# Kernel optimization log

Hardware: AMD Instinct MI355X
Metric: run time of the kernel (lower is better)

The kernel has to match this reference:

```python
import jax, jax.numpy as jnp
import numpy as np

H, W, C = 64, 64, 64
B = 64
N_HEADS = 4
CONV_FILTERS = 64
BASIS_DIM = 16


def get_spatial_basis(h, w, d):
    half_d = d // 2
    basis = np.zeros((h, w, d), dtype=np.float32)
    div = np.exp(np.arange(0, half_d, 2, dtype=np.float32) * -np.log(100.0) / half_d)
    h_grid = np.expand_dims(np.arange(0, h, dtype=np.float32), 1)
    w_grid = np.expand_dims(np.arange(0, w, dtype=np.float32), 1)
    basis[:, :, 0:half_d:2] = np.sin(h_grid * div)[:, np.newaxis, :]
    basis[:, :, 1:half_d:2] = np.cos(h_grid * div)[:, np.newaxis, :]
    basis[:, :, half_d::2] = np.sin(w_grid * div)[np.newaxis, :, :]
    basis[:, :, half_d + 1::2] = np.cos(w_grid * div)[np.newaxis, :, :]
    return basis


def setup_inputs() -> dict:
    key = jax.random.key(0)
    ks = jax.random.split(key, 8)
    feat_in = C + BASIS_DIM  # 80 input channels for 1x1 convs
    return {
        "image": jax.random.normal(ks[0], (B, H, W, C), jnp.float32),
        "state1": jax.random.normal(ks[1], (B, 512), jnp.float32),
        "state2": jax.random.normal(ks[2], (B, 512), jnp.float32),
        "extra": jax.random.normal(ks[3], (B, 256), jnp.float32),
        "Wq": jax.random.normal(ks[4], (1024, CONV_FILTERS), jnp.float32) * 0.03,
        "bq": jnp.zeros((CONV_FILTERS,), jnp.float32),
        "Wk": jax.random.normal(ks[5], (feat_in, CONV_FILTERS), jnp.float32) * 0.1,
        "bk": jnp.zeros((CONV_FILTERS,), jnp.float32),
        "Wv": jax.random.normal(ks[6], (feat_in, CONV_FILTERS), jnp.float32) * 0.1,
        "bv": jnp.zeros((CONV_FILTERS,), jnp.float32),
        "spatial_basis": jnp.asarray(get_spatial_basis(H, W, BASIS_DIM)),
    }


def reference(image, state1, state2, extra, Wq, bq, Wk, bk, Wv, bv, spatial_basis):
    b, h, w, _ = image.shape
    nh = N_HEADS
    cf = Wq.shape[1]
    dph = cf // nh  # depth per head

    # concat image with tiled spatial basis -> [B,h,w,C+basis_dim]
    sb = jnp.broadcast_to(spatial_basis[None], (b,) + spatial_basis.shape)
    feats = jnp.concatenate([image, sb], axis=-1)

    # combiner over network-state tensors, then Dense query
    state = jnp.concatenate([state1, state2], axis=-1)  # [B,1024]
    q = state @ Wq + bq                                 # [B,cf]

    # 1x1 convs == per-pixel dense projections
    keys = feats @ Wk + bk    # [B,h,w,cf]
    vals = feats @ Wv + bv    # [B,h,w,cf]

    qh = q.reshape(b, nh, dph)
    kh = keys.reshape(b, h * w, nh, dph)
    vh = vals.reshape(b, h * w, nh, dph)

    # per-head dot scores over spatial positions, softmax over positions
    scores = jnp.einsum('bnd,bpnd->bpn', qh, kh)        # [B,hw,nh]
    attn = jax.nn.softmax(scores, axis=1)
    mean_attn = attn.mean(axis=-1).reshape(b, h, w)

    # weighted sum of values over spatial positions -> [B,cf]
    pooled = jnp.einsum('bpn,bpnd->bnd', attn, vh).reshape(b, cf)

    out = jnp.concatenate([pooled, extra], axis=-1)
    return out, mean_attn
```

## Files before the change

### kernel.cpp

```cpp
#include <hip/hip_runtime.h>
#include <hip/hip_bf16.h>

#define BATCH 64
#define HW    4096
#define PT    128
#define NS    32
#define FT_ST 136

#define FT_BASE  0
#define EST_BASE 10880
#define PR_BASE  13056
#define RED_BASE 15616
#define SMEM_TOT 15680

typedef unsigned int u32;
typedef unsigned short u16;
typedef __attribute__((ext_vector_type(8))) short bf16x8;
typedef __attribute__((ext_vector_type(4))) float f32x4;

__device__ __forceinline__ float bf2f(u16 h) { return __uint_as_float(((u32)h) << 16); }
__device__ __forceinline__ u32 f2bf(float x) {
  u32 b = __float_as_uint(x);
  return (b + 0x7fffu + ((b >> 16) & 1u)) >> 16;
}
__device__ __forceinline__ u32 pkbf(float lo, float hi) { return f2bf(lo) | (f2bf(hi) << 16); }

template<bool F32>
__device__ __forceinline__ float ld(const void* p, size_t i) {
  if (F32) return ((const float*)p)[i];
  return bf2f(((const u16*)p)[i]);
}
template<bool F32>
__device__ __forceinline__ void st(void* p, size_t i, float v) {
  if (F32) ((float*)p)[i] = v;
  else     ((__hip_bfloat16*)p)[i] = __float2bfloat16(v);
}

__device__ __forceinline__ bool detect_f32(const u16* __restrict__ image) {
  u16 h = image[(threadIdx.x & 63) * 2];
  u32 e = (h >> 7) & 0xFFu;
  unsigned long long m = __ballot(e >= 0x86u);
  return __popcll(m) >= 8;
}

__device__ __forceinline__ int swz(int c) { return ((c >> 3) & 3) << 3; }

template<bool F32>
__device__ void k1_body(const void* state1, const void* state2, const void* Wq, const void* bq,
                        const void* Wk, const void* bk, u16* weffbt, float* cb,
                        float* stt, float* qp, float* q) {
  const int b = blockIdx.x, tid = threadIdx.x;
  for (int i = tid; i < 512; i += 256) {
    stt[i]       = ld<F32>(state1, (size_t)b * 512 + i);
    stt[512 + i] = ld<F32>(state2, (size_t)b * 512 + i);
  }
  u32* wz = (u32*)(weffbt + (size_t)b * 1664);
  for (int i = tid; i < 832; i += 256) wz[i] = 0u;
  __syncthreads();
  {
    const int j = tid & 63, g = tid >> 6, i0 = g * 256;
    float a = 0.f;
#pragma unroll 8
    for (int i = 0; i < 256; ++i) a += stt[i0 + i] * ld<F32>(Wq, (size_t)(i0 + i) * 64 + j);
    qp[g * 64 + j] = a;
  }
  __syncthreads();
  if (tid < 64) q[tid] = qp[tid] + qp[64 + tid] + qp[128 + tid] + qp[192 + tid] + ld<F32>(bq, tid);
  __syncthreads();
  for (int t = tid; t < 320; t += 256) {
    const int c = t >> 2, n = t & 3;
    float a = 0.f;
#pragma unroll
    for (int d = 0; d < 16; ++d) a += ld<F32>(Wk, (size_t)c * 64 + n * 16 + d) * q[n * 16 + d];
    weffbt[(size_t)b * 1664 + n * 104 + c] = (u16)f2bf(a);
  }
  if (tid < 4) {
    float a = 0.f;
#pragma unroll
    for (int d = 0; d < 16; ++d) a += ld<F32>(bk, tid * 16 + d) * q[tid * 16 + d];
    cb[b * 4 + tid] = a;
  }
}

__global__ __launch_bounds__(256) void k1_prep(
    const void* image, const void* state1, const void* state2, const void* Wq, const void* bq,
    const void* Wk, const void* bk, u16* weffbt, float* cb) {
  __shared__ float stt[1024];
  __shared__ float qp[256];
  __shared__ float q[64];
  if (detect_f32((const u16*)image))
       k1_body<true >(state1, state2, Wq, bq, Wk, bk, weffbt, cb, stt, qp, q);
  else k1_body<false>(state1, state2, Wq, bq, Wk, bk, weffbt, cb, stt, qp, q);
}

__global__ __launch_bounds__(256, 4) void k2_main(
    const void* __restrict__ image, const void* __restrict__ basis,
    const float* __restrict__ cb, const u16* __restrict__ weffbt,
    u16* __restrict__ e_buf, float* __restrict__ m_blk, float* __restrict__ sum_blk,
    float* __restrict__ fpool_part) {
  __shared__ __align__(16) u16 smem[SMEM_TOT];
  float* redf  = (float*)(smem + RED_BASE);
  float* red2f = (float*)(smem + RED_BASE + 32);

  const int tid = threadIdx.x;
  const int b = blockIdx.x & 63, s = blockIdx.x >> 6;
  const int bs = b * NS + s;
  const int wave = tid >> 6, lane = tid & 63;
  const int m = lane & 15, q = lane >> 4;
  const bool isf32 = detect_f32((const u16*)image);

  if (isf32) {
    const float4* img4 = (const float4*)image + ((size_t)(b * HW + s * PT)) * 16;
#pragma unroll
    for (int i = 0; i < 4; ++i) {
      const int fidx = i * 256 + tid;
      const int pq = fidx >> 4, c4 = fidx & 15;
      const int ps = (pq * 2) ^ (((c4 >> 1) & 3) << 3);
      float4 v0 = img4[(pq * 2) * 16 + c4];
      float4 v1 = img4[(pq * 2 + 1) * 16 + c4];
      *(u32*)&smem[FT_BASE + (c4 * 4 + 0) * FT_ST + ps] = pkbf(v0.x, v1.x);
      *(u32*)&smem[FT_BASE + (c4 * 4 + 1) * FT_ST + ps] = pkbf(v0.y, v1.y);
      *(u32*)&smem[FT_BASE + (c4 * 4 + 2) * FT_ST + ps] = pkbf(v0.z, v1.z);
      *(u32*)&smem[FT_BASE + (c4 * 4 + 3) * FT_ST + ps] = pkbf(v0.w, v1.w);
    }
    const float4* bas4 = (const float4*)basis + (size_t)(s * PT) * 4;
    {
      const int pq = tid >> 2, c4 = tid & 3;
      const int ps = (pq * 2) ^ (((c4 >> 1) & 3) << 3);
      float4 v0 = bas4[(pq * 2) * 4 + c4];
      float4 v1 = bas4[(pq * 2 + 1) * 4 + c4];
      *(u32*)&smem[FT_BASE + (64 + c4 * 4 + 0) * FT_ST + ps] = pkbf(v0.x, v1.x);
      *(u32*)&smem[FT_BASE + (64 + c4 * 4 + 1) * FT_ST + ps] = pkbf(v0.y, v1.y);
      *(u32*)&smem[FT_BASE + (64 + c4 * 4 + 2) * FT_ST + ps] = pkbf(v0.z, v1.z);
      *(u32*)&smem[FT_BASE + (64 + c4 * 4 + 3) * FT_ST + ps] = pkbf(v0.w, v1.w);
    }
  } else {
    const uint4* img4 = (const uint4*)image + ((size_t)(b * HW + s * PT)) * 8;
#pragma unroll
    for (int i = 0; i < 2; ++i) {
      const int fidx = i * 256 + tid;
      const int pq = fidx >> 3, c8 = fidx & 7;
      const int ps = (pq * 2) ^ ((c8 & 3) << 3);
      uint4 u0 = img4[(pq * 2) * 8 + c8];
      uint4 u1 = img4[(pq * 2 + 1) * 8 + c8];
      const u32 w0[4] = {u0.x, u0.y, u0.z, u0.w};
      const u32 w1[4] = {u1.x, u1.y, u1.z, u1.w};
#pragma unroll
      for (int k = 0; k < 4; ++k) {
        *(u32*)&smem[FT_BASE + (c8 * 8 + 2 * k) * FT_ST + ps]     = (w0[k] & 0xffffu) | (w1[k] << 16);
        *(u32*)&smem[FT_BASE + (c8 * 8 + 2 * k + 1) * FT_ST + ps] = (w0[k] >> 16) | (w1[k] & 0xffff0000u);
      }
    }
    const uint4* bas4 = (const uint4*)basis + (size_t)(s * PT) * 2;
    if (tid < 128) {
      const int pq = tid >> 1, c8 = tid & 1;
      const int ps = (pq * 2) ^ ((c8 & 3) << 3);
      uint4 u0 = bas4[(pq * 2) * 2 + c8];
      uint4 u1 = bas4[(pq * 2 + 1) * 2 + c8];
      const u32 w0[4] = {u0.x, u0.y, u0.z, u0.w};
      const u32 w1[4] = {u1.x, u1.y, u1.z, u1.w};
#pragma unroll
      for (int k = 0; k < 4; ++k) {
        *(u32*)&smem[FT_BASE + (64 + c8 * 8 + 2 * k) * FT_ST + ps]     = (w0[k] & 0xffffu) | (w1[k] << 16);
        *(u32*)&smem[FT_BASE + (64 + c8 * 8 + 2 * k + 1) * FT_ST + ps] = (w0[k] >> 16) | (w1[k] & 0xffff0000u);
      }
    }
  }
  bf16x8 bfr[3];
  {
    const u16* wrow = weffbt + (size_t)b * 1664 + m * 104;
#pragma unroll
    for (int s3 = 0; s3 < 3; ++s3) bfr[s3] = *(const bf16x8*)&wrow[s3 * 32 + q * 8];
  }
  __syncthreads();

  f32x4 accS[2];
  {
    const float ci = (m < 4) ? cb[b * 4 + m] : 0.f;
#pragma unroll
    for (int t = 0; t < 2; ++t) { accS[t][0] = ci; accS[t][1] = ci; accS[t][2] = ci; accS[t][3] = ci; }
#pragma unroll
    for (int t = 0; t < 2; ++t) {
      const int pos = (wave * 2 + t) * 16 + m;
#pragma unroll
      for (int s3 = 0; s3 < 3; ++s3) {
        u32 aw[4];
        if (s3 == 2 && q >= 2) {
          aw[0] = aw[1] = aw[2] = aw[3] = 0u;
        } else {
#pragma unroll
          for (int jp = 0; jp < 4; ++jp) {
            const int c0 = s3 * 32 + q * 8 + jp * 2;
            const int ps = pos ^ swz(c0);
            u32 lo = smem[FT_BASE + c0 * FT_ST + ps];
            u32 hi = smem[FT_BASE + (c0 + 1) * FT_ST + ps];
            aw[jp] = lo | (hi << 16);
          }
        }
        accS[t] = __builtin_amdgcn_mfma_f32_16x16x32_bf16(*(const bf16x8*)aw, bfr[s3], accS[t], 0, 0, 0);
      }
    }
  }
  {
    float mx = accS[0][0];
#pragma unroll
    for (int t = 0; t < 2; ++t)
#pragma unroll
      for (int r = 0; r < 4; ++r) mx = fmaxf(mx, accS[t][r]);
    mx = fmaxf(mx, __shfl_xor(mx, 16, 64));
    mx = fmaxf(mx, __shfl_xor(mx, 32, 64));
    if (lane < 4) redf[wave * 4 + lane] = mx;
  }
  __syncthreads();

  float bmv;
  {
    const int hh = m & 3;
    bmv = fmaxf(fmaxf(redf[hh], redf[4 + hh]), fmaxf(redf[8 + hh], redf[12 + hh]));
  }
  {
    float ss = 0.f;
#pragma unroll
    for (int t = 0; t < 2; ++t) {
      const int T = wave * 2 + t;
#pragma unroll
      for (int r = 0; r < 4; ++r) {
        float e = __expf(accS[t][r] - bmv);
        u32 eb = f2bf(e);
        ss += bf2f((u16)eb);
        if (m < 4) smem[EST_BASE + m * FT_ST + T * 16 + q * 4 + r] = (u16)eb;
      }
    }
    ss += __shfl_xor(ss, 16, 64);
    ss += __shfl_xor(ss, 32, 64);
    if (lane < 4) red2f[wave * 4 + lane] = ss;
  }
  __syncthreads();

  if (tid < 4) {
    const int hh = tid;
    m_blk[bs * 4 + hh] = fmaxf(fmaxf(redf[hh], redf[4 + hh]), fmaxf(redf[8 + hh], redf[12 + hh]));
    sum_blk[bs * 4 + hh] = red2f[hh] + red2f[4 + hh] + red2f[8 + hh] + red2f[12 + hh];
  }
  {
    const int n = tid >> 6, pp = tid & 63;
    u32 v = *(const u32*)&smem[EST_BASE + n * FT_ST + pp * 2];
    ((u32*)e_buf)[((size_t)(b * 4 + n)) * 2048 + s * 64 + pp] = v;
  }
  {
    bf16x8 ap = *(const bf16x8*)&smem[EST_BASE + m * FT_ST + wave * 32 + q * 8];
    f32x4 accP[5];
#pragma unroll
    for (int T = 0; T < 5; ++T) { accP[T][0] = 0; accP[T][1] = 0; accP[T][2] = 0; accP[T][3] = 0; }
#pragma unroll
    for (int T = 0; T < 5; ++T) {
      const int c = T * 16 + m;
      const int g = (wave * 32 + q * 8) ^ swz(c);
      bf16x8 bp = *(const bf16x8*)&smem[FT_BASE + c * FT_ST + g];
      accP[T] = __builtin_amdgcn_mfma_f32_16x16x32_bf16(ap, bp, accP[T], 0, 0, 0);
    }
    if (lane < 16) {
      float* pr = (float*)(smem + PR_BASE);
#pragma unroll
      for (int T = 0; T < 5; ++T)
#pragma unroll
        for (int r = 0; r < 4; ++r)
          pr[((wave * 5 + T) * 4 + r) * 16 + lane] = accP[T][r];
    }
  }
  __syncthreads();
  {
    const float* pr = (const float*)(smem + PR_BASE);
    for (int t = tid; t < 320; t += 256) {
      const int n = t / 80, c = t - n * 80;
      const int tile = c >> 4, cc = c & 15;
      float a = 0.f;
#pragma unroll
      for (int w = 0; w < 4; ++w) a += pr[((w * 5 + tile) * 4 + n) * 16 + cc];
      fpool_part[(size_t)bs * 320 + t] = a;
    }
  }
}

template<bool F32>
__device__ void k34_body(const float* m_blk, const float* sum_blk, const u16* e_buf,
                         const float* fpool_part, const void* Wv, const void* bv,
                         const void* extra, void* out, float* esc, float* fp) {
  const int tid = threadIdx.x;
  const int b = blockIdx.x & 63, s16 = blockIdx.x >> 6;
  if (tid < 4) {
    float M = -3.4e38f;
#pragma unroll
    for (int sp = 0; sp < NS; ++sp) M = fmaxf(M, m_blk[(b * NS + sp) * 4 + tid]);
    float den = 0.f;
#pragma unroll
    for (int sp = 0; sp < NS; ++sp)
      den += __expf(m_blk[(b * NS + sp) * 4 + tid] - M) * sum_blk[(b * NS + sp) * 4 + tid];
    float rd = 1.0f / den;
#pragma unroll
    for (int sp = 0; sp < NS; ++sp)
      esc[sp * 4 + tid] = __expf(m_blk[(b * NS + sp) * 4 + tid] - M) * rd;
  }
  __syncthreads();
  {
    const int gpos = s16 * 256 + tid;
    const int s32 = gpos >> 7;
    float mean = 0.f;
#pragma unroll
    for (int n = 0; n < 4; ++n)
      mean += bf2f(e_buf[(size_t)(b * 4 + n) * HW + gpos]) * esc[s32 * 4 + n];
    st<F32>(out, (size_t)BATCH * 320 + (size_t)b * HW + gpos, 0.25f * mean);
  }
  if (s16 == 0) {
    for (int idx = tid; idx < 320; idx += 256) {
      const int n2 = idx / 80;
      float a = 0.f;
#pragma unroll
      for (int sp = 0; sp < NS; ++sp)
        a += esc[sp * 4 + n2] * fpool_part[(size_t)(b * NS + sp) * 320 + idx];
      fp[idx] = a;
    }
    __syncthreads();
    if (tid < 64) {
      const int n = tid >> 4;
      float dot = 0.f;
#pragma unroll
      for (int c = 0; c < 80; ++c) dot += fp[n * 80 + c] * ld<F32>(Wv, (size_t)c * 64 + tid);
      st<F32>(out, (size_t)b * 320 + tid, dot + ld<F32>(bv, tid));
    }
    st<F32>(out, (size_t)b * 320 + 64 + tid, ld<F32>(extra, (size_t)b * 256 + tid));
  }
}

__global__ __launch_bounds__(256) void k34_out(
    const void* image, const float* m_blk, const float* sum_blk, const u16* e_buf,
    const float* fpool_part, const void* Wv, const void* bv, const void* extra, void* out) {
  __shared__ float esc[NS * 4];
  __shared__ float fp[320];
  if (detect_f32((const u16*)image))
       k34_body<true >(m_blk, sum_blk, e_buf, fpool_part, Wv, bv, extra, out, esc, fp);
  else k34_body<false>(m_blk, sum_blk, e_buf, fpool_part, Wv, bv, extra, out, esc, fp);
}

extern "C" void kernel_launch(void* const* d_in, const int* in_sizes, int n_in,
                              void* d_out, int out_size, void* d_ws, size_t ws_size,
                              hipStream_t stream) {
  (void)in_sizes; (void)n_in; (void)out_size; (void)ws_size;
  const void* image  = d_in[0];
  const void* state1 = d_in[1];
  const void* state2 = d_in[2];
  const void* extra  = d_in[3];
  const void* Wq = d_in[4];
  const void* bq = d_in[5];
  const void* Wk = d_in[6];
  const void* bk = d_in[7];
  const void* Wv = d_in[8];
  const void* bv = d_in[9];
  const void* basis = d_in[10];

  float* ws         = (float*)d_ws;
  float* cb         = ws;
  float* m_blk      = ws + 256;
  float* sum_blk    = ws + 8448;
  float* fpool_part = ws + 16640;
  u16*   weffbt     = (u16*)(ws + 672000);
  u16*   e_buf      = (u16*)(ws + 725248);

  k1_prep<<<dim3(BATCH), dim3(256), 0, stream>>>(image, state1, state2, Wq, bq, Wk, bk, weffbt, cb);
  k2_main<<<dim3(BATCH * NS), dim3(256), 0, stream>>>(image, basis, cb, weffbt,
                                                      e_buf, m_blk, sum_blk, fpool_part);
  k34_out<<<dim3(BATCH * 16), dim3(256), 0, stream>>>(image, m_blk, sum_blk, e_buf,
                                                      fpool_part, Wv, bv, extra, d_out);
}
```

Measured before the change: 131.7 us.

## Store features as channel-pair-packed u32 rows in shared memory

Changes the shared-memory feature tile from one channel per row of bf16 positions to a layout where each u32 holds a channel pair for one position, with a new row swizzle. Global loads become contiguous single float4/uint4 per pixel, and the score MFMA operand gathers become single 32-bit LDS reads instead of two 16-bit reads plus shifts. The pooling MFMA now needs byte-permute instructions and wider LDS reads to extract one channel from the pairs, and f32 packing uses the paired bf16 conversion intrinsic.

```diff
diff --git a/kernel.cpp b/kernel.cpp
--- a/kernel.cpp
+++ b/kernel.cpp
@@ -6,12 +6,12 @@
 #define PT    128
 #define NS    32
 #define FT_ST 136
-
-#define FT_BASE  0
-#define EST_BASE 10880
-#define PR_BASE  13056
-#define RED_BASE 15616
-#define SMEM_TOT 15680
+#define CP_ST 132
+
+#define EST_BASE 10560
+#define PR_BASE  12736
+#define RED_BASE 15296
+#define SMEM_U32 7680
 
 typedef unsigned int u32;
 typedef unsigned short u16;
@@ -23,7 +23,10 @@
   u32 b = __float_as_uint(x);
   return (b + 0x7fffu + ((b >> 16) & 1u)) >> 16;
 }
-__device__ __forceinline__ u32 pkbf(float lo, float hi) { return f2bf(lo) | (f2bf(hi) << 16); }
+__device__ __forceinline__ u32 pk2(float lo, float hi) {
+  __hip_bfloat162 h = __float22bfloat162_rn(make_float2(lo, hi));
+  u32 r; __builtin_memcpy(&r, &h, 4); return r;
+}
 
 template<bool F32>
 __device__ __forceinline__ float ld(const void* p, size_t i) {
@@ -43,7 +46,7 @@
   return __popcll(m) >= 8;
 }
 
-__device__ __forceinline__ int swz(int c) { return ((c >> 3) & 3) << 3; }
+__device__ __forceinline__ int swr(int r) { return ((r >> 2) & 3) << 3; }
 
 template<bool F32>
 __device__ void k1_body(const void* state1, const void* state2, const void* Wq, const void* bq,
@@ -98,7 +101,9 @@
     const float* __restrict__ cb, const u16* __restrict__ weffbt,
     u16* __restrict__ e_buf, float* __restrict__ m_blk, float* __restrict__ sum_blk,
     float* __restrict__ fpool_part) {
-  __shared__ __align__(16) u16 smem[SMEM_TOT];
+  __shared__ __align__(16) u32 smem32[SMEM_U32];
+  u16* smem = (u16*)smem32;
+  u32* cpi = smem32;
   float* redf  = (float*)(smem + RED_BASE);
   float* red2f = (float*)(smem + RED_BASE + 32);
 
@@ -112,58 +117,48 @@
   if (isf32) {
     const float4* img4 = (const float4*)image + ((size_t)(b * HW + s * PT)) * 16;
 #pragma unroll
+    for (int i = 0; i < 8; ++i) {
+      const int fidx = i * 256 + tid;
+      const int p = fidx >> 4, c4 = fidx & 15;
+      float4 v = img4[fidx];
+      const int r0 = c4 * 2, sw = swr(r0);
+      cpi[r0 * CP_ST + (p ^ sw)]        = pk2(v.x, v.y);
+      cpi[(r0 + 1) * CP_ST + (p ^ sw)]  = pk2(v.z, v.w);
+    }
+    const float4* bas4 = (const float4*)basis + (size_t)(s * PT) * 4;
+#pragma unroll
+    for (int i = 0; i < 2; ++i) {
+      const int fidx = i * 256 + tid;
+      const int p = fidx >> 2, c4 = fidx & 3;
+      float4 v = bas4[fidx];
+      const int r0 = 32 + c4 * 2, sw = swr(r0);
+      cpi[r0 * CP_ST + (p ^ sw)]        = pk2(v.x, v.y);
+      cpi[(r0 + 1) * CP_ST + (p ^ sw)]  = pk2(v.z, v.w);
+    }
+  } else {
+    const uint4* img4 = (const uint4*)image + ((size_t)(b * HW + s * PT)) * 8;
+#pragma unroll
     for (int i = 0; i < 4; ++i) {
       const int fidx = i * 256 + tid;
-      const int pq = fidx >> 4, c4 = fidx & 15;
-      const int ps = (pq * 2) ^ (((c4 >> 1) & 3) << 3);
-      float4 v0 = img4[(pq * 2) * 16 + c4];
-      float4 v1 = img4[(pq * 2 + 1) * 16 + c4];
-      *(u32*)&smem[FT_BASE + (c4 * 4 + 0) * FT_ST + ps] = pkbf(v0.x, v1.x);
-      *(u32*)&smem[FT_BASE + (c4 * 4 + 1) * FT_ST + ps] = pkbf(v0.y, v1.y);
-      *(u32*)&smem[FT_BASE + (c4 * 4 + 2) * FT_ST + ps] = pkbf(v0.z, v1.z);
-      *(u32*)&smem[FT_BASE + (c4 * 4 + 3) * FT_ST + ps] = pkbf(v0.w, v1.w);
-    }
-    const float4* bas4 = (const float4*)basis + (size_t)(s * PT) * 4;
+      const int p = fidx >> 3, c8 = fidx & 7;
+      uint4 u = img4[fidx];
+      const int rb = c8 * 4;
+      const int base = rb * CP_ST + (p ^ swr(rb));
+      cpi[base]              = u.x;
+      cpi[base + CP_ST]      = u.y;
+      cpi[base + 2 * CP_ST]  = u.z;
+      cpi[base + 3 * CP_ST]  = u.w;
+    }
+    const uint4* bas4 = (const uint4*)basis + (size_t)(s * PT) * 2;
     {
-      const int pq = tid >> 2, c4 = tid & 3;
-      const int ps = (pq * 2) ^ (((c4 >> 1) & 3) << 3);
-      float4 v0 = bas4[(pq * 2) * 4 + c4];
-      float4 v1 = bas4[(pq * 2 + 1) * 4 + c4];
-      *(u32*)&smem[FT_BASE + (64 + c4 * 4 + 0) * FT_ST + ps] = pkbf(v0.x, v1.x);
-      *(u32*)&smem[FT_BASE + (64 + c4 * 4 + 1) * FT_ST + ps] = pkbf(v0.y, v1.y);
-      *(u32*)&smem[FT_BASE + (64 + c4 * 4 + 2) * FT_ST + ps] = pkbf(v0.z, v1.z);
-      *(u32*)&smem[FT_BASE + (64 + c4 * 4 + 3) * FT_ST + ps] = pkbf(v0.w, v1.w);
-    }
-  } else {
-    const uint4* img4 = (const uint4*)image + ((size_t)(b * HW + s * PT)) * 8;
-#pragma unroll
-    for (int i = 0; i < 2; ++i) {
-      const int fidx = i * 256 + tid;
-      const int pq = fidx >> 3, c8 = fidx & 7;
-      const int ps = (pq * 2) ^ ((c8 & 3) << 3);
-      uint4 u0 = img4[(pq * 2) * 8 + c8];
-      uint4 u1 = img4[(pq * 2 + 1) * 8 + c8];
-      const u32 w0[4] = {u0.x, u0.y, u0.z, u0.w};
-      const u32 w1[4] = {u1.x, u1.y, u1.z, u1.w};
-#pragma unroll
-      for (int k = 0; k < 4; ++k) {
-        *(u32*)&smem[FT_BASE + (c8 * 8 + 2 * k) * FT_ST + ps]     = (w0[k] & 0xffffu) | (w1[k] << 16);
-        *(u32*)&smem[FT_BASE + (c8 * 8 + 2 * k + 1) * FT_ST + ps] = (w0[k] >> 16) | (w1[k] & 0xffff0000u);
-      }
-    }
-    const uint4* bas4 = (const uint4*)basis + (size_t)(s * PT) * 2;
-    if (tid < 128) {
-      const int pq = tid >> 1, c8 = tid & 1;
-      const int ps = (pq * 2) ^ ((c8 & 3) << 3);
-      uint4 u0 = bas4[(pq * 2) * 2 + c8];
-      uint4 u1 = bas4[(pq * 2 + 1) * 2 + c8];
-      const u32 w0[4] = {u0.x, u0.y, u0.z, u0.w};
-      const u32 w1[4] = {u1.x, u1.y, u1.z, u1.w};
-#pragma unroll
-      for (int k = 0; k < 4; ++k) {
-        *(u32*)&smem[FT_BASE + (64 + c8 * 8 + 2 * k) * FT_ST + ps]     = (w0[k] & 0xffffu) | (w1[k] << 16);
-        *(u32*)&smem[FT_BASE + (64 + c8 * 8 + 2 * k + 1) * FT_ST + ps] = (w0[k] >> 16) | (w1[k] & 0xffff0000u);
-      }
+      const int p = tid >> 1, c8 = tid & 1;
+      uint4 u = bas4[tid];
+      const int rb = 32 + c8 * 4;
+      const int base = rb * CP_ST + (p ^ swr(rb));
+      cpi[base]              = u.x;
+      cpi[base + CP_ST]      = u.y;
+      cpi[base + 2 * CP_ST]  = u.z;
+      cpi[base + 3 * CP_ST]  = u.w;
     }
   }
   bf16x8 bfr[3];
@@ -182,20 +177,16 @@
 #pragma unroll
     for (int t = 0; t < 2; ++t) {
       const int pos = (wave * 2 + t) * 16 + m;
+      const int psw = pos ^ (q << 3);
 #pragma unroll
       for (int s3 = 0; s3 < 3; ++s3) {
         u32 aw[4];
         if (s3 == 2 && q >= 2) {
           aw[0] = aw[1] = aw[2] = aw[3] = 0u;
         } else {
-#pragma unroll
-          for (int jp = 0; jp < 4; ++jp) {
-            const int c0 = s3 * 32 + q * 8 + jp * 2;
-            const int ps = pos ^ swz(c0);
-            u32 lo = smem[FT_BASE + c0 * FT_ST + ps];
-            u32 hi = smem[FT_BASE + (c0 + 1) * FT_ST + ps];
-            aw[jp] = lo | (hi << 16);
-          }
+          const int rbase = s3 * 16 + q * 4;
+#pragma unroll
+          for (int jp = 0; jp < 4; ++jp) aw[jp] = cpi[(rbase + jp) * CP_ST + psw];
         }
         accS[t] = __builtin_amdgcn_mfma_f32_16x16x32_bf16(*(const bf16x8*)aw, bfr[s3], accS[t], 0, 0, 0);
       }
@@ -255,9 +246,17 @@
 #pragma unroll
     for (int T = 0; T < 5; ++T) {
       const int c = T * 16 + m;
-      const int g = (wave * 32 + q * 8) ^ swz(c);
-      bf16x8 bp = *(const bf16x8*)&smem[FT_BASE + c * FT_ST + g];
-      accP[T] = __builtin_amdgcn_mfma_f32_16x16x32_bf16(ap, bp, accP[T], 0, 0, 0);
+      const int r = c >> 1;
+      const u32 sel = (c & 1) ? 0x07060302u : 0x05040100u;
+      const int p0 = (wave * 32 + q * 8) ^ swr(r);
+      const uint4* w01 = (const uint4*)&cpi[r * CP_ST + p0];
+      uint4 wa = w01[0], wb = w01[1];
+      u32 bw[4];
+      bw[0] = __builtin_amdgcn_perm(wa.y, wa.x, sel);
+      bw[1] = __builtin_amdgcn_perm(wa.w, wa.z, sel);
+      bw[2] = __builtin_amdgcn_perm(wb.y, wb.x, sel);
+      bw[3] = __builtin_amdgcn_perm(wb.w, wb.z, sel);
+      accP[T] = __builtin_amdgcn_mfma_f32_16x16x32_bf16(ap, *(const bf16x8*)bw, accP[T], 0, 0, 0);
     }
     if (lane < 16) {
       float* pr = (float*)(smem + PR_BASE);
```

New measurement: 130.8 us. About the same (-0.7%).
